# Kernel tuning notes

Hardware: AMD Instinct MI355X
Metric: run time of the kernel (lower is better)

Reference implementation:

```python
import jax, jax.numpy as jnp
import numpy as np

VOCAB = 50257
HID = 1024
B, T = 8, 256

def setup_inputs() -> dict:
    key = jax.random.key(0)
    ks = jax.random.split(key, 6)
    initrange = 0.1
    emb_W = jax.random.uniform(ks[0], (VOCAB, HID), jnp.float32, -initrange, initrange)
    # PyTorch LSTM default init: U(-1/sqrt(H), 1/sqrt(H))
    s = 1.0 / np.sqrt(HID)
    w_ih = jax.random.uniform(ks[1], (4 * HID, HID), jnp.float32, -s, s)
    w_hh = jax.random.uniform(ks[2], (4 * HID, HID), jnp.float32, -s, s)
    b_ih = jax.random.uniform(ks[3], (4 * HID,), jnp.float32, -s, s)
    b_hh = jax.random.uniform(ks[4], (4 * HID,), jnp.float32, -s, s)
    dec_b = jnp.zeros((VOCAB,), jnp.float32)
    x = jax.random.randint(ks[5], (B, T), 0, VOCAB, dtype=jnp.int32)
    return {"x": x, "emb_W": emb_W, "w_ih": w_ih, "w_hh": w_hh,
            "b_ih": b_ih, "b_hh": b_hh, "dec_b": dec_b}

def _lstm(emb, w_ih, w_hh, b_ih, b_hh):
    # emb: [B, T, H] -> outputs [B, T, H], final (h, c) each [1, B, H]
    Bq, Tq, H = emb.shape
    # precompute input projections for all timesteps: [T, B, 4H]
    x_proj = jnp.einsum('bth,gh->tbg', emb, w_ih) + (b_ih + b_hh)
    h0 = jnp.zeros((Bq, H), emb.dtype)
    c0 = jnp.zeros((Bq, H), emb.dtype)

    def step(carry, xp):
        h, c = carry
        gates = xp + h @ w_hh.T                     # [B, 4H]
        i, f, g, o = jnp.split(gates, 4, axis=-1)   # PyTorch gate order i,f,g,o
        i = jax.nn.sigmoid(i)
        f = jax.nn.sigmoid(f)
        g = jnp.tanh(g)
        o = jax.nn.sigmoid(o)
        c = f * c + i * g
        h = o * jnp.tanh(c)
        return (h, c), h

    (hT, cT), hs = jax.lax.scan(step, (h0, c0), x_proj)
    out = jnp.transpose(hs, (1, 0, 2))              # [B, T, H]
    return out, (hT[None], cT[None])

def reference(x, emb_W, w_ih, w_hh, b_ih, b_hh, dec_b):
    emb = emb_W[x]                                  # [B, T, H] (dropout in eval mode = identity)
    out, hidden = _lstm(emb, w_ih, w_hh, b_ih, b_hh)
    logits = jnp.einsum('bth,vh->btv', out, emb_W) + dec_b   # tied decoder weight
    logits = logits.reshape(-1, VOCAB)              # [B*T, V]
    return jax.nn.log_softmax(logits, axis=1), hidden
```

## Files before the change

kernel.cpp:

```cpp
#include <hip/hip_runtime.h>

typedef short bf16x8 __attribute__((ext_vector_type(8)));
typedef float f32x4 __attribute__((ext_vector_type(4)));

#define HID   1024
#define BATCH 8
#define TLEN  256
#define VOCABN 50257
#define GATES 4096
#define M_ROWS 2048

__device__ __forceinline__ unsigned short f2bf(float x) {
  unsigned int u = __float_as_uint(x);
  unsigned int r = (u + 0x7fffu + ((u >> 16) & 1u)) >> 16;
  return (unsigned short)r;
}

__device__ __forceinline__ unsigned agent_load(const unsigned* p) {
  return __hip_atomic_load(p, __ATOMIC_RELAXED, __HIP_MEMORY_SCOPE_AGENT);
}
__device__ __forceinline__ unsigned long long agent_load64(const unsigned long long* p) {
  return __hip_atomic_load(p, __ATOMIC_RELAXED, __HIP_MEMORY_SCOPE_AGENT);
}
__device__ __forceinline__ void agent_store(unsigned* p, unsigned v) {
  __hip_atomic_store(p, v, __ATOMIC_RELAXED, __HIP_MEMORY_SCOPE_AGENT);
}

__global__ void conv_f32_bf16(const float* __restrict__ src,
                              unsigned short* __restrict__ dst, int n4) {
  int i = blockIdx.x * 256 + threadIdx.x;
  if (i >= n4) return;
  float4 v = ((const float4*)src)[i];
  ushort4 o;
  o.x = f2bf(v.x); o.y = f2bf(v.y); o.z = f2bf(v.z); o.w = f2bf(v.w);
  ((ushort4*)dst)[i] = o;
}

__global__ void bias_sum_kernel(const float* __restrict__ a,
                                const float* __restrict__ b,
                                float* __restrict__ o) {
  int i = blockIdx.x * 256 + threadIdx.x;
  if (i < GATES) o[i] = a[i] + b[i];
}

__global__ void init_flags(unsigned* __restrict__ f) {
  f[blockIdx.x * 256 + threadIdx.x] = 0u;
}

#define GSTR 72

__global__ __launch_bounds__(256) void gemm_bt_bf16(
    const unsigned short* __restrict__ A, const unsigned short* __restrict__ Bm,
    const float* __restrict__ bias, float* __restrict__ C,
    const int* __restrict__ tokens, int ldc, int Nreal) {
  __shared__ unsigned short As[128 * GSTR];
  __shared__ unsigned short Bs[128 * GSTR];
  const int tid = threadIdx.x;
  const int m0 = blockIdx.x * 128;
  const int n0 = blockIdx.y * 128;
  const int wid = tid >> 6, lane = tid & 63;
  const int wm = (wid & 1) * 64, wn = (wid >> 1) * 64;
  const int lm = lane & 15, quad = lane >> 4;

  f32x4 acc[4][4];
  #pragma unroll
  for (int i = 0; i < 4; ++i)
    #pragma unroll
    for (int j = 0; j < 4; ++j) acc[i][j] = (f32x4){0.f, 0.f, 0.f, 0.f};

  for (int k0 = 0; k0 < HID; k0 += 64) {
    #pragma unroll
    for (int it = 0; it < 4; ++it) {
      int c = tid + it * 256;
      int row = c >> 3, ch = c & 7;
      int gm = m0 + row;
      int arow = tokens ? tokens[gm] : gm;
      uint4 v = *(const uint4*)(A + (size_t)arow * HID + k0 + ch * 8);
      *(uint4*)&As[row * GSTR + ch * 8] = v;
      int gn = n0 + row;
      uint4 w = make_uint4(0u, 0u, 0u, 0u);
      if (gn < Nreal) w = *(const uint4*)(Bm + (size_t)gn * HID + k0 + ch * 8);
      *(uint4*)&Bs[row * GSTR + ch * 8] = w;
    }
    __syncthreads();
    #pragma unroll
    for (int kk = 0; kk < 2; ++kk) {
      bf16x8 af[4], bfr[4];
      #pragma unroll
      for (int i = 0; i < 4; ++i)
        af[i] = *(const bf16x8*)&As[(wm + i * 16 + lm) * GSTR + kk * 32 + quad * 8];
      #pragma unroll
      for (int j = 0; j < 4; ++j)
        bfr[j] = *(const bf16x8*)&Bs[(wn + j * 16 + lm) * GSTR + kk * 32 + quad * 8];
      #pragma unroll
      for (int i = 0; i < 4; ++i)
        #pragma unroll
        for (int j = 0; j < 4; ++j)
          acc[i][j] = __builtin_amdgcn_mfma_f32_16x16x32_bf16(af[i], bfr[j], acc[i][j], 0, 0, 0);
    }
    __syncthreads();
  }
  #pragma unroll
  for (int i = 0; i < 4; ++i) {
    #pragma unroll
    for (int j = 0; j < 4; ++j) {
      #pragma unroll
      for (int r = 0; r < 4; ++r) {
        int gm = m0 + wm + i * 16 + quad * 4 + r;
        int gn = n0 + wn + j * 16 + lm;
        if (gn < Nreal)
          C[(size_t)gm * ldc + gn] = acc[i][j][r] + (bias ? bias[gn] : 0.f);
      }
    }
  }
}

__global__ __launch_bounds__(256) void lstm_persistent(
    const float* __restrict__ whh, const float* __restrict__ xproj,
    float* __restrict__ hbuf, unsigned short* __restrict__ adec,
    float* __restrict__ out_hc, unsigned* __restrict__ flags) {
  __shared__ float smem[1024 * 9];
  __shared__ float gsum[16][8];
  const int tid = threadIdx.x;
  const int lane = tid & 63;
  const int rq = tid >> 6;
  const int j0 = blockIdx.x * 4;

  float wreg[4][16];
  #pragma unroll
  for (int i = 0; i < 4; ++i)
    #pragma unroll
    for (int kk = 0; kk < 16; ++kk)
      wreg[i][kk] = whh[(size_t)(i * HID + j0 + rq) * HID + kk * 64 + lane];

  const int ur = tid >> 3, ub = tid & 7;
  const int ui = ur & 3, uq = ur >> 2;
  float creg = 0.f;

  unsigned* grp  = flags + (blockIdx.x >> 4) * 16;
  unsigned* root = flags + 512;

  for (int t = 0; t < TLEN; ++t) {
    float xp = 0.f;
    if (tid < 128)
      xp = xproj[(size_t)(ub * TLEN + t) * GATES + ui * HID + j0 + uq];

    const unsigned long long* hsrc =
        (const unsigned long long*)(hbuf + (size_t)(t & 1) * (BATCH * HID));
    if (t > 0) {
      #pragma unroll
      for (int it = 0; it < 16; ++it) {
        int c = tid + it * 256;
        unsigned long long v = agent_load64(&hsrc[c]);
        int k = c >> 2, off = (c & 3) * 2;
        smem[k * 9 + off]     = __uint_as_float((unsigned)v);
        smem[k * 9 + off + 1] = __uint_as_float((unsigned)(v >> 32));
      }
    } else {
      #pragma unroll
      for (int it = 0; it < 16; ++it) {
        int c = tid + it * 256;
        int k = c >> 2, off = (c & 3) * 2;
        smem[k * 9 + off] = 0.f;
        smem[k * 9 + off + 1] = 0.f;
      }
    }
    __syncthreads();

    float acc[4][8];
    #pragma unroll
    for (int i = 0; i < 4; ++i)
      #pragma unroll
      for (int b = 0; b < 8; ++b) acc[i][b] = 0.f;
    #pragma unroll
    for (int kk = 0; kk < 16; ++kk) {
      const float* hp = &smem[(kk * 64 + lane) * 9];
      float4 ha = *(const float4*)hp;
      float4 hb = *(const float4*)(hp + 4);
      #pragma unroll
      for (int i = 0; i < 4; ++i) {
        float w = wreg[i][kk];
        acc[i][0] += w * ha.x; acc[i][1] += w * ha.y;
        acc[i][2] += w * ha.z; acc[i][3] += w * ha.w;
        acc[i][4] += w * hb.x; acc[i][5] += w * hb.y;
        acc[i][6] += w * hb.z; acc[i][7] += w * hb.w;
      }
    }
    __syncthreads();

    #pragma unroll
    for (int i = 0; i < 4; ++i)
      #pragma unroll
      for (int b = 0; b < 8; ++b)
        smem[(size_t)(i * 8 + b) * 257 + tid] = acc[i][b];
    __syncthreads();

    if (tid < 128) {
      const float* rp = &smem[(size_t)(ui * 8 + ub) * 257 + uq * 64];
      float s0 = 0.f, s1 = 0.f, s2 = 0.f, s3 = 0.f;
      #pragma unroll
      for (int c = 0; c < 16; ++c) {
        s0 += rp[c * 4 + 0]; s1 += rp[c * 4 + 1];
        s2 += rp[c * 4 + 2]; s3 += rp[c * 4 + 3];
      }
      gsum[ur][ub] = (s0 + s1) + (s2 + s3) + xp;
    }
    __syncthreads();

    if (tid < 32) {
      const int cl = tid >> 3, bb = tid & 7, j = j0 + cl;
      float gi = gsum[cl * 4 + 0][bb];
      float gf = gsum[cl * 4 + 1][bb];
      float gg = gsum[cl * 4 + 2][bb];
      float go = gsum[cl * 4 + 3][bb];
      float si = 1.f / (1.f + __expf(-gi));
      float sf = 1.f / (1.f + __expf(-gf));
      float tg = tanhf(gg);
      float so = 1.f / (1.f + __expf(-go));
      float c = sf * creg + si * tg;
      creg = c;
      float h = so * tanhf(c);
      agent_store((unsigned*)&hbuf[(size_t)((t + 1) & 1) * (BATCH * HID) + j * 8 + bb],
                  __float_as_uint(h));
      adec[(size_t)(bb * TLEN + t) * HID + j] = f2bf(h);
      if (t == TLEN - 1) {
        out_hc[bb * HID + j] = h;
        out_hc[BATCH * HID + bb * HID + j] = c;
      }
    }

    if (t + 1 < TLEN) {
      __syncthreads();
      if (tid == 0) {
        unsigned prev = __hip_atomic_fetch_add(grp, 1u, __ATOMIC_RELAXED,
                                               __HIP_MEMORY_SCOPE_AGENT);
        if ((prev & 15u) == 15u)
          __hip_atomic_fetch_add(root, 1u, __ATOMIC_RELAXED,
                                 __HIP_MEMORY_SCOPE_AGENT);
        unsigned target = (unsigned)(t + 1) * 16u;
        while (agent_load(root) < target) __builtin_amdgcn_s_sleep(1);
      }
      __syncthreads();
    }
  }
}

__global__ __launch_bounds__(512) void logsoftmax_rows(float* __restrict__ data) {
  const int row = blockIdx.x;
  float* p = data + (size_t)row * VOCABN;
  const int tid = threadIdx.x;
  float m = -INFINITY, l = 0.f;
  for (int i = tid; i < VOCABN; i += 512) {
    float x = p[i];
    float nm = fmaxf(m, x);
    l = l * __expf(m - nm) + __expf(x - nm);
    m = nm;
  }
  #pragma unroll
  for (int off = 32; off > 0; off >>= 1) {
    float m2 = __shfl_down(m, off);
    float l2 = __shfl_down(l, off);
    float nm = fmaxf(m, m2);
    l = l * __expf(m - nm) + l2 * __expf(m2 - nm);
    m = nm;
  }
  __shared__ float sm[8], sl[8];
  if ((tid & 63) == 0) { sm[tid >> 6] = m; sl[tid >> 6] = l; }
  __syncthreads();
  if (tid == 0) {
    m = sm[0]; l = sl[0];
    for (int i2 = 1; i2 < 8; ++i2) {
      float m2 = sm[i2], l2 = sl[i2];
      float nm = fmaxf(m, m2);
      l = l * __expf(m - nm) + l2 * __expf(m2 - nm);
      m = nm;
    }
    sm[0] = m; sl[0] = logf(l);
  }
  __syncthreads();
  float M = sm[0], L = sl[0];
  for (int i = tid; i < VOCABN; i += 512) p[i] = p[i] - M - L;
}

extern "C" void kernel_launch(void* const* d_in, const int* in_sizes, int n_in,
                              void* d_out, int out_size, void* d_ws, size_t ws_size,
                              hipStream_t stream) {
  const int*   x     = (const int*)d_in[0];
  const float* embW  = (const float*)d_in[1];
  const float* w_ih  = (const float*)d_in[2];
  const float* w_hh  = (const float*)d_in[3];
  const float* b_ih  = (const float*)d_in[4];
  const float* b_hh  = (const float*)d_in[5];
  const float* dec_b = (const float*)d_in[6];
  float* out = (float*)d_out;

  char* ws = (char*)d_ws;
  unsigned short* emb_bf = (unsigned short*)ws;  ws += (size_t)VOCABN * HID * 2;
  unsigned short* wih_bf = (unsigned short*)ws;  ws += (size_t)GATES * HID * 2;
  float* bias_s = (float*)ws;                    ws += (size_t)GATES * 4;
  float* xproj  = (float*)ws;                    ws += (size_t)M_ROWS * GATES * 4;
  unsigned short* adec = (unsigned short*)ws;    ws += (size_t)M_ROWS * HID * 2;
  float* hbuf = (float*)ws;                      ws += (size_t)2 * BATCH * HID * 4;
  unsigned* flags = (unsigned*)ws;               ws += 4096;

  int n4emb = VOCABN * HID / 4;
  conv_f32_bf16<<<(n4emb + 255) / 256, 256, 0, stream>>>(embW, emb_bf, n4emb);
  int n4wih = GATES * HID / 4;
  conv_f32_bf16<<<(n4wih + 255) / 256, 256, 0, stream>>>(w_ih, wih_bf, n4wih);
  bias_sum_kernel<<<16, 256, 0, stream>>>(b_ih, b_hh, bias_s);
  init_flags<<<4, 256, 0, stream>>>(flags);

  gemm_bt_bf16<<<dim3(16, 32), 256, 0, stream>>>(emb_bf, wih_bf, bias_s, xproj,
                                                 x, GATES, GATES);

  float* out_hc = out + (size_t)M_ROWS * VOCABN;
  void* kargs[] = {(void*)&w_hh, (void*)&xproj, (void*)&hbuf,
                   (void*)&adec, (void*)&out_hc, (void*)&flags};
  hipError_t ce = hipLaunchCooperativeKernel((void*)lstm_persistent,
                                             dim3(256), dim3(256), kargs, 0, stream);
  if (ce != hipSuccess) {
    lstm_persistent<<<dim3(256), dim3(256), 0, stream>>>(w_hh, xproj, hbuf,
                                                         adec, out_hc, flags);
  }

  gemm_bt_bf16<<<dim3(16, 393), 256, 0, stream>>>(adec, emb_bf, dec_b, out,
                                                  nullptr, VOCABN, VOCABN);

  logsoftmax_rows<<<2048, 512, 0, stream>>>(out);
}
```

Baseline: 4.862 ms.

## Replace grid-wide counter barrier with NaN-sentinel dataflow sync on hidden state

Removes the two-level atomic counter barrier between LSTM timesteps. Each block now spins directly on the hidden-state values, which are pre-filled with a NaN sentinel, in a 16-slot ring buffer, and one rotating block resets a consumed slot back to the sentinel. This cuts the per-step barrier round trip and lets blocks proceed as soon as their inputs arrive. The cost is polling on 4096 64-bit words per block and reliance on relaxed-ordering visibility. A genuine NaN in h, or a slot reset racing with slow readers, could hang or corrupt the result.

Result: faster. 4.159 ms (-14.4%).

```diff
diff --git a/kernel.cpp b/kernel.cpp
--- a/kernel.cpp
+++ b/kernel.cpp
@@ -9,6 +9,8 @@
 #define VOCABN 50257
 #define GATES 4096
 #define M_ROWS 2048
+#define HSLOTS 16
+#define SENT 0x7fc00000u
 
 __device__ __forceinline__ unsigned short f2bf(float x) {
   unsigned int u = __float_as_uint(x);
@@ -16,9 +18,6 @@
   return (unsigned short)r;
 }
 
-__device__ __forceinline__ unsigned agent_load(const unsigned* p) {
-  return __hip_atomic_load(p, __ATOMIC_RELAXED, __HIP_MEMORY_SCOPE_AGENT);
-}
 __device__ __forceinline__ unsigned long long agent_load64(const unsigned long long* p) {
   return __hip_atomic_load(p, __ATOMIC_RELAXED, __HIP_MEMORY_SCOPE_AGENT);
 }
@@ -43,8 +42,11 @@
   if (i < GATES) o[i] = a[i] + b[i];
 }
 
-__global__ void init_flags(unsigned* __restrict__ f) {
-  f[blockIdx.x * 256 + threadIdx.x] = 0u;
+__global__ void init_hseq(float* __restrict__ hseq) {
+  int i = blockIdx.x * 256 + threadIdx.x;
+  unsigned fill = ((i * 4) < BATCH * HID) ? 0u : SENT;
+  uint4 v = make_uint4(fill, fill, fill, fill);
+  ((uint4*)hseq)[i] = v;
 }
 
 #define GSTR 72
@@ -117,8 +119,8 @@
 
 __global__ __launch_bounds__(256) void lstm_persistent(
     const float* __restrict__ whh, const float* __restrict__ xproj,
-    float* __restrict__ hbuf, unsigned short* __restrict__ adec,
-    float* __restrict__ out_hc, unsigned* __restrict__ flags) {
+    float* __restrict__ hseq, unsigned short* __restrict__ adec,
+    float* __restrict__ out_hc) {
   __shared__ float smem[1024 * 9];
   __shared__ float gsum[16][8];
   const int tid = threadIdx.x;
@@ -137,35 +139,37 @@
   const int ui = ur & 3, uq = ur >> 2;
   float creg = 0.f;
 
-  unsigned* grp  = flags + (blockIdx.x >> 4) * 16;
-  unsigned* root = flags + 512;
-
   for (int t = 0; t < TLEN; ++t) {
     float xp = 0.f;
     if (tid < 128)
       xp = xproj[(size_t)(ub * TLEN + t) * GATES + ui * HID + j0 + uq];
 
     const unsigned long long* hsrc =
-        (const unsigned long long*)(hbuf + (size_t)(t & 1) * (BATCH * HID));
-    if (t > 0) {
-      #pragma unroll
-      for (int it = 0; it < 16; ++it) {
-        int c = tid + it * 256;
-        unsigned long long v = agent_load64(&hsrc[c]);
-        int k = c >> 2, off = (c & 3) * 2;
-        smem[k * 9 + off]     = __uint_as_float((unsigned)v);
-        smem[k * 9 + off + 1] = __uint_as_float((unsigned)(v >> 32));
-      }
-    } else {
-      #pragma unroll
-      for (int it = 0; it < 16; ++it) {
-        int c = tid + it * 256;
-        int k = c >> 2, off = (c & 3) * 2;
-        smem[k * 9 + off] = 0.f;
-        smem[k * 9 + off + 1] = 0.f;
-      }
-    }
-    __syncthreads();
+        (const unsigned long long*)(hseq + (size_t)(t & (HSLOTS - 1)) * (BATCH * HID));
+    unsigned long long v[16];
+    #pragma unroll
+    for (int it = 0; it < 16; ++it)
+      v[it] = agent_load64(&hsrc[tid + it * 256]);
+    #pragma unroll
+    for (int it = 0; it < 16; ++it) {
+      unsigned long long x = v[it];
+      while ((unsigned)x == SENT || (unsigned)(x >> 32) == SENT) {
+        __builtin_amdgcn_s_sleep(1);
+        x = agent_load64(&hsrc[tid + it * 256]);
+      }
+      int c = tid + it * 256;
+      int k = c >> 2, off = (c & 3) * 2;
+      smem[k * 9 + off]     = __uint_as_float((unsigned)x);
+      smem[k * 9 + off + 1] = __uint_as_float((unsigned)(x >> 32));
+    }
+    __syncthreads();
+
+    if (t >= 1 && ((unsigned)(t - 1) & 255u) == blockIdx.x) {
+      unsigned* ps = (unsigned*)(hseq + (size_t)((t - 1) & (HSLOTS - 1)) * (BATCH * HID));
+      #pragma unroll
+      for (int it = 0; it < 32; ++it)
+        agent_store(&ps[tid + it * 256], SENT);
+    }
 
     float acc[4][8];
     #pragma unroll
@@ -220,28 +224,16 @@
       float c = sf * creg + si * tg;
       creg = c;
       float h = so * tanhf(c);
-      agent_store((unsigned*)&hbuf[(size_t)((t + 1) & 1) * (BATCH * HID) + j * 8 + bb],
-                  __float_as_uint(h));
+      if (t + 1 < TLEN)
+        agent_store((unsigned*)&hseq[(size_t)((t + 1) & (HSLOTS - 1)) * (BATCH * HID) + j * 8 + bb],
+                    __float_as_uint(h));
       adec[(size_t)(bb * TLEN + t) * HID + j] = f2bf(h);
       if (t == TLEN - 1) {
         out_hc[bb * HID + j] = h;
         out_hc[BATCH * HID + bb * HID + j] = c;
       }
     }
-
-    if (t + 1 < TLEN) {
-      __syncthreads();
-      if (tid == 0) {
-        unsigned prev = __hip_atomic_fetch_add(grp, 1u, __ATOMIC_RELAXED,
-                                               __HIP_MEMORY_SCOPE_AGENT);
-        if ((prev & 15u) == 15u)
-          __hip_atomic_fetch_add(root, 1u, __ATOMIC_RELAXED,
-                                 __HIP_MEMORY_SCOPE_AGENT);
-        unsigned target = (unsigned)(t + 1) * 16u;
-        while (agent_load(root) < target) __builtin_amdgcn_s_sleep(1);
-      }
-      __syncthreads();
-    }
+    __syncthreads();
   }
 }
 
@@ -300,27 +292,26 @@
   float* bias_s = (float*)ws;                    ws += (size_t)GATES * 4;
   float* xproj  = (float*)ws;                    ws += (size_t)M_ROWS * GATES * 4;
   unsigned short* adec = (unsigned short*)ws;    ws += (size_t)M_ROWS * HID * 2;
-  float* hbuf = (float*)ws;                      ws += (size_t)2 * BATCH * HID * 4;
-  unsigned* flags = (unsigned*)ws;               ws += 4096;
+  float* hseq = (float*)ws;                      ws += (size_t)HSLOTS * BATCH * HID * 4;
 
   int n4emb = VOCABN * HID / 4;
   conv_f32_bf16<<<(n4emb + 255) / 256, 256, 0, stream>>>(embW, emb_bf, n4emb);
   int n4wih = GATES * HID / 4;
   conv_f32_bf16<<<(n4wih + 255) / 256, 256, 0, stream>>>(w_ih, wih_bf, n4wih);
   bias_sum_kernel<<<16, 256, 0, stream>>>(b_ih, b_hh, bias_s);
-  init_flags<<<4, 256, 0, stream>>>(flags);
+  init_hseq<<<HSLOTS * BATCH * HID / 1024, 256, 0, stream>>>(hseq);
 
   gemm_bt_bf16<<<dim3(16, 32), 256, 0, stream>>>(emb_bf, wih_bf, bias_s, xproj,
                                                  x, GATES, GATES);
 
   float* out_hc = out + (size_t)M_ROWS * VOCABN;
-  void* kargs[] = {(void*)&w_hh, (void*)&xproj, (void*)&hbuf,
-                   (void*)&adec, (void*)&out_hc, (void*)&flags};
+  void* kargs[] = {(void*)&w_hh, (void*)&xproj, (void*)&hseq,
+                   (void*)&adec, (void*)&out_hc};
   hipError_t ce = hipLaunchCooperativeKernel((void*)lstm_persistent,
                                              dim3(256), dim3(256), kargs, 0, stream);
   if (ce != hipSuccess) {
-    lstm_persistent<<<dim3(256), dim3(256), 0, stream>>>(w_hh, xproj, hbuf,
-                                                         adec, out_hc, flags);
+    lstm_persistent<<<dim3(256), dim3(256), 0, stream>>>(w_hh, xproj, hseq,
+                                                         adec, out_hc);
   }
 
   gemm_bt_bf16<<<dim3(16, 393), 256, 0, stream>>>(adec, emb_bf, dec_b, out,
```
